# Optimization experiments

Measured on AMD Instinct MI355X. Metric: run time of the kernel, lower is better.

Reference implementation:

```python
import jax, jax.numpy as jnp
import numpy as np

B, R, SR, K, F = 1, 2048, 24, 8, 32
DIST_FREQ = 2   # dist_xyz_freq -> PE dim 2*2*3 = 12
VIEW_FREQ = 4   # num_viewdir_freqs -> PE dim 2*4*3 = 24


def pe(x, n_freqs):
    # positional encoding: concat sin/cos of x * 2^i, flattened over last dim
    fb = (2.0 ** jnp.arange(n_freqs)).astype(x.dtype)          # [L]
    xb = x[..., None] * fb                                      # [..., 3, L]
    enc = jnp.concatenate([jnp.sin(xb), jnp.cos(xb)], axis=-1)  # [..., 3, 2L]
    return enc.reshape(*x.shape[:-1], -1)                       # [..., 3*2L]


def setup_inputs() -> dict:
    key = jax.random.key(0)
    ks = jax.random.split(key, 12)
    s = 0.1  # small init scale for weights
    return {
        'sampled_embedding': jax.random.normal(ks[0], (B, R, SR, K, F), jnp.float32),
        'dists': jax.random.normal(ks[1], (B, R, SR, K, 3), jnp.float32) * 0.1,
        'viewdirs': jax.random.normal(ks[2], (B, R, SR, 3), jnp.float32),
        'pnt_mask': jax.random.randint(ks[3], (B, R, SR, K), 0, 2, jnp.int32),
        'w1': jax.random.normal(ks[4], (F + 2 * DIST_FREQ * 3, 256), jnp.float32) * s,
        'b1': jnp.zeros((256,), jnp.float32),
        'w2': jax.random.normal(ks[5], (256, 256), jnp.float32) * s,
        'b2': jnp.zeros((256,), jnp.float32),
        'wa1': jax.random.normal(ks[6], (256, 256), jnp.float32) * s,
        'ba1': jnp.zeros((256,), jnp.float32),
        'wa2': jax.random.normal(ks[7], (256, 1), jnp.float32) * s,
        'ba2': jnp.zeros((1,), jnp.float32),
        'wc1': jax.random.normal(ks[8], (256 + 2 * VIEW_FREQ * 3, 256), jnp.float32) * s,
        'bc1': jnp.zeros((256,), jnp.float32),
        'wc2': jax.random.normal(ks[9], (256, 3), jnp.float32) * s,
        'bc2': jnp.zeros((3,), jnp.float32),
    }


def reference(sampled_embedding, dists, viewdirs, pnt_mask,
              w1, b1, w2, b2, wa1, ba1, wa2, ba2, wc1, bc1, wc2, bc2):
    mask = pnt_mask.astype(sampled_embedding.dtype)             # [B,R,SR,K]

    # quadric distance kernel -> normalized neighbor weights
    d2 = jnp.sum(dists * dists, axis=-1)                        # [B,R,SR,K]
    w = 1.0 / jnp.clip(d2, 1e-8)
    w = w * mask
    w = w / jnp.clip(jnp.sum(w, axis=-1, keepdims=True), 1e-8)  # agg_weight_norm

    # per-neighbor feature MLP (block1): feat ++ PE(dist_xyz) -> 256 -> 256
    feat_in = jnp.concatenate([sampled_embedding, pe(dists, DIST_FREQ)], axis=-1)
    h = jax.nn.relu(feat_in @ w1 + b1)
    h = jax.nn.relu(h @ w2 + b2)                                # [B,R,SR,K,256]

    # distance-weighted aggregation over neighbors (apply_pnt_mask folded into w)
    agg = jnp.einsum('brsk,brskc->brsc', w, h)                  # [B,R,SR,256]

    # alpha branch + raw2out_density (act_super: softplus(raw - 1))
    ah = jax.nn.relu(agg @ wa1 + ba1)
    density = jax.nn.softplus(ah @ wa2 + ba2 - 1.0)             # [B,R,SR,1]

    # color branch + raw2out_color (widened sigmoid)
    cin = jnp.concatenate([agg, pe(viewdirs, VIEW_FREQ)], axis=-1)
    ch = jax.nn.relu(cin @ wc1 + bc1)
    color = jax.nn.sigmoid(ch @ wc2 + bc2) * (1.0 + 2e-3) - 1e-3  # [B,R,SR,3]

    return jnp.concatenate([density, color], axis=-1)           # [B,R,SR,4]
```

## Files before the change

### kernel.cpp

```cpp
#include <hip/hip_runtime.h>

typedef unsigned short ushort_t;
typedef __bf16 bf16x8 __attribute__((ext_vector_type(8)));
typedef float f32x4 __attribute__((ext_vector_type(4)));

#define NPTS   49152
#define KNBR   8
#define PTS_A  8
#define NBLK_A (NPTS / PTS_A)
#define PTS_B  32
#define NBLK_B (NPTS / PTS_B)

#define W1S_OFF   0
#define W2S_OFF   16384
#define WA1S_OFF  81920
#define WC1S_OFF  147456
#define WA2S_OFF  221184
#define WC2S_OFF  225280
#define WS_WEIGHT 229376
#define AGG_OFF   229376

__device__ __forceinline__ float b2f(ushort_t u) {
    return __builtin_bit_cast(float, ((unsigned)u) << 16);
}
__device__ __forceinline__ ushort_t f2b(float f) {
    unsigned x = __builtin_bit_cast(unsigned, f);
    unsigned r = x + 0x7fffu + ((x >> 16) & 1u);
    return (ushort_t)(r >> 16);
}
__device__ __forceinline__ ushort_t f2bc(float f) {
    unsigned x = __builtin_bit_cast(unsigned, f);
    return (ushort_t)((x + 0x8000u) >> 16);
}

__global__ __launch_bounds__(256) void prep_swizzle(
    const float* __restrict__ w1, const float* __restrict__ w2,
    const float* __restrict__ wa1, const float* __restrict__ wc1,
    const float* __restrict__ wa2, const float* __restrict__ wc2,
    ushort_t* __restrict__ ws)
{
    int idx = blockIdx.x * 256 + threadIdx.x;
    if (idx >= WS_WEIGHT) return;

    if (idx >= WA2S_OFF) {
        int off2 = idx - WA2S_OFF;
        int mat = off2 >> 12;
        int off = off2 & 4095;
        int kb = off >> 7, rem = off & 127;
        int n = rem >> 3, j = rem & 7;
        int k = kb * 8 + j;
        float v = 0.f;
        if (mat == 0) { if (n == 0) v = wa2[k]; }
        else          { if (n < 3)  v = wc2[k * 3 + n]; }
        ws[idx] = f2b(v);
        return;
    }

    const float* src; int off, srcK, base;
    if (idx < W2S_OFF)        { src = w1;  base = W1S_OFF;  off = idx - W1S_OFF;  srcK = 44;  }
    else if (idx < WA1S_OFF)  { src = w2;  base = W2S_OFF;  off = idx - W2S_OFF;  srcK = 256; }
    else if (idx < WC1S_OFF)  { src = wa1; base = WA1S_OFF; off = idx - WA1S_OFF; srcK = 256; }
    else                      { src = wc1; base = WC1S_OFF; off = idx - WC1S_OFF; srcK = 280; }
    int kb  = off >> 11;
    int rem = off & 2047;
    int j = rem >> 8;
    int n = rem & 255;
    int k = kb * 8 + j;
    float v = (k < srcK) ? src[k * 256 + n] : 0.f;
    ws[base + kb * 2048 + n * 8 + j] = f2b(v);
}

__global__ __launch_bounds__(256) void pa_mlp(
    const float* __restrict__ emb, const float* __restrict__ dists,
    const int* __restrict__ mask,  const float* __restrict__ b1,
    const float* __restrict__ b2,  const ushort_t* __restrict__ ws,
    ushort_t* __restrict__ aggg)
{
    __shared__ __align__(16) ushort_t uH1[64 * 264];
    __shared__ __align__(16) float sWraw[64];
    __shared__ __align__(16) float sWn[64];
    ushort_t (*sFeat)[72] = (ushort_t(*)[72])uH1;
    ushort_t (*sH1)[264]  = (ushort_t(*)[264])uH1;

    const int tid  = threadIdx.x;
    const int lane = tid & 63;
    const int wv   = tid >> 6;
    const int n0   = lane & 15;
    const int quad = lane >> 4;
    const int pb   = blockIdx.x * PTS_A;
    const int colB = wv * 64;

    {
        int g0 = blockIdx.x * 2048 + tid * 8;
        int r = tid >> 2, c8 = (tid & 3) * 8;
        float4 f0 = *(const float4*)(emb + g0);
        float4 f1 = *(const float4*)(emb + g0 + 4);
        ushort_t v8[8];
        v8[0] = f2bc(f0.x); v8[1] = f2bc(f0.y); v8[2] = f2bc(f0.z); v8[3] = f2bc(f0.w);
        v8[4] = f2bc(f1.x); v8[5] = f2bc(f1.y); v8[6] = f2bc(f1.z); v8[7] = f2bc(f1.w);
        *(uint4*)&sFeat[r][c8] = *(uint4*)v8;
    }
    if (tid < 64) {
        int gr = pb * KNBR + tid;
        float x = dists[gr * 3 + 0];
        float y = dists[gr * 3 + 1];
        float z = dists[gr * 3 + 2];
        float d2 = x * x + y * y + z * z;
        sWraw[tid] = (float)mask[gr] / fmaxf(d2, 1e-8f);
        float xs[3] = {x, y, z};
        #pragma unroll
        for (int d = 0; d < 3; d++) {
            #pragma unroll
            for (int l = 0; l < 2; l++) {
                float ang = xs[d] * (float)(1 << l);
                sFeat[tid][32 + d * 4 + l]     = f2bc(__sinf(ang));
                sFeat[tid][32 + d * 4 + 2 + l] = f2bc(__cosf(ang));
            }
        }
        #pragma unroll
        for (int c = 44; c < 64; c++) sFeat[tid][c] = 0;
    }
    __syncthreads();
    if (tid < 64) {
        int lp = tid >> 3;
        float s = 0.f;
        #pragma unroll
        for (int k = 0; k < 8; k++) s += sWraw[lp * 8 + k];
        sWn[tid] = sWraw[tid] / fmaxf(s, 1e-8f);
    }

    f32x4 acc[16];
    #pragma unroll
    for (int i = 0; i < 16; i++) acc[i] = (f32x4){0.f, 0.f, 0.f, 0.f};

    #pragma unroll
    for (int ki = 0; ki < 2; ki++) {
        bf16x8 a[4];
        #pragma unroll
        for (int mt = 0; mt < 4; mt++)
            a[mt] = *(const bf16x8*)&sFeat[mt * 16 + n0][ki * 32 + quad * 8];
        const ushort_t* bp = ws + W1S_OFF + ki * 8192 + quad * 2048 + (colB + n0) * 8;
        #pragma unroll
        for (int nt = 0; nt < 4; nt++) {
            bf16x8 b = *(const bf16x8*)(bp + nt * 128);
            #pragma unroll
            for (int mt = 0; mt < 4; mt++)
                acc[mt * 4 + nt] = __builtin_amdgcn_mfma_f32_16x16x32_bf16(a[mt], b, acc[mt * 4 + nt], 0, 0, 0);
        }
    }
    __syncthreads();

    {
        #pragma unroll
        for (int nt = 0; nt < 4; nt++) {
            int col = colB + nt * 16 + n0;
            float bias = b1[col];
            #pragma unroll
            for (int mt = 0; mt < 4; mt++)
                #pragma unroll
                for (int r = 0; r < 4; r++)
                    sH1[mt * 16 + quad * 4 + r][col] = f2bc(fmaxf(acc[mt * 4 + nt][r] + bias, 0.f));
        }
    }
    __syncthreads();

    #pragma unroll
    for (int i = 0; i < 16; i++) acc[i] = (f32x4){0.f, 0.f, 0.f, 0.f};
    #pragma unroll
    for (int ki = 0; ki < 8; ki++) {
        bf16x8 a[4];
        #pragma unroll
        for (int mt = 0; mt < 4; mt++)
            a[mt] = *(const bf16x8*)&sH1[mt * 16 + n0][ki * 32 + quad * 8];
        const ushort_t* bp = ws + W2S_OFF + ki * 8192 + quad * 2048 + (colB + n0) * 8;
        #pragma unroll
        for (int nt = 0; nt < 4; nt++) {
            bf16x8 b = *(const bf16x8*)(bp + nt * 128);
            #pragma unroll
            for (int mt = 0; mt < 4; mt++)
                acc[mt * 4 + nt] = __builtin_amdgcn_mfma_f32_16x16x32_bf16(a[mt], b, acc[mt * 4 + nt], 0, 0, 0);
        }
    }
    {
        #pragma unroll
        for (int mt = 0; mt < 4; mt++) {
            f32x4 wn4 = *(const f32x4*)&sWn[mt * 16 + quad * 4];
            #pragma unroll
            for (int nt = 0; nt < 4; nt++) {
                int col = colB + nt * 16 + n0;
                float bias = b2[col];
                float s = fmaxf(acc[mt * 4 + nt][0] + bias, 0.f) * wn4[0]
                        + fmaxf(acc[mt * 4 + nt][1] + bias, 0.f) * wn4[1]
                        + fmaxf(acc[mt * 4 + nt][2] + bias, 0.f) * wn4[2]
                        + fmaxf(acc[mt * 4 + nt][3] + bias, 0.f) * wn4[3];
                s += __shfl_xor(s, 16);
                if ((quad & 1) == 0) {
                    int pt = pb + 2 * mt + (quad >> 1);
                    aggg[(size_t)pt * 256 + col] = f2bc(s);
                }
            }
        }
    }
}

__global__ __launch_bounds__(256) void pa_branch(
    const float* __restrict__ vdirs,
    const float* __restrict__ ba1v, const float* __restrict__ ba2v,
    const float* __restrict__ bc1v, const float* __restrict__ bc2v,
    const ushort_t* __restrict__ ws, const ushort_t* __restrict__ aggg,
    float* __restrict__ out)
{
    __shared__ __align__(16) ushort_t reg1[32 * 296];
    __shared__ __align__(16) ushort_t reg2[32 * 264];
    ushort_t (*sCin)[296] = (ushort_t(*)[296])reg1;
    ushort_t (*sAh)[264]  = (ushort_t(*)[264])reg1;
    ushort_t (*sCh)[264]  = (ushort_t(*)[264])reg2;

    const int tid  = threadIdx.x;
    const int lane = tid & 63;
    const int wv   = tid >> 6;
    const int n0   = lane & 15;
    const int quad = lane >> 4;
    const int pb   = blockIdx.x * PTS_B;
    const int colB = wv * 64;

    #pragma unroll
    for (int it = 0; it < 4; it++) {
        int idx = (tid + it * 256) * 8;
        uint4 v = *(const uint4*)(aggg + (size_t)pb * 256 + idx);
        *(uint4*)&sCin[idx >> 8][idx & 255] = v;
    }
    #pragma unroll
    for (int it = 0; it < 3; it++) {
        int t = tid + it * 256;
        int p = t / 24, j = t % 24;
        int d = j >> 3, jj = j & 7, l = jj & 3, isc = jj >> 2;
        float ang = vdirs[(pb + p) * 3 + d] * (float)(1 << l);
        sCin[p][256 + j] = f2bc(isc ? __cosf(ang) : __sinf(ang));
    }
    sCin[tid >> 3][280 + (tid & 7)] = 0;
    __syncthreads();

    f32x4 accA[8], accC[8];
    #pragma unroll
    for (int i = 0; i < 8; i++) { accA[i] = (f32x4){0.f, 0.f, 0.f, 0.f}; accC[i] = accA[i]; }

    #pragma unroll
    for (int ki = 0; ki < 8; ki++) {
        bf16x8 a0 = *(const bf16x8*)&sCin[n0][ki * 32 + quad * 8];
        bf16x8 a1 = *(const bf16x8*)&sCin[16 + n0][ki * 32 + quad * 8];
        const ushort_t* bp = ws + WA1S_OFF + ki * 8192 + quad * 2048 + (colB + n0) * 8;
        #pragma unroll
        for (int nt = 0; nt < 4; nt++) {
            bf16x8 b = *(const bf16x8*)(bp + nt * 128);
            accA[nt]     = __builtin_amdgcn_mfma_f32_16x16x32_bf16(a0, b, accA[nt], 0, 0, 0);
            accA[4 + nt] = __builtin_amdgcn_mfma_f32_16x16x32_bf16(a1, b, accA[4 + nt], 0, 0, 0);
        }
    }
    #pragma unroll
    for (int ki = 0; ki < 9; ki++) {
        bf16x8 a0 = *(const bf16x8*)&sCin[n0][ki * 32 + quad * 8];
        bf16x8 a1 = *(const bf16x8*)&sCin[16 + n0][ki * 32 + quad * 8];
        const ushort_t* bp = ws + WC1S_OFF + ki * 8192 + quad * 2048 + (colB + n0) * 8;
        #pragma unroll
        for (int nt = 0; nt < 4; nt++) {
            bf16x8 b = *(const bf16x8*)(bp + nt * 128);
            accC[nt]     = __builtin_amdgcn_mfma_f32_16x16x32_bf16(a0, b, accC[nt], 0, 0, 0);
            accC[4 + nt] = __builtin_amdgcn_mfma_f32_16x16x32_bf16(a1, b, accC[4 + nt], 0, 0, 0);
        }
    }
    __syncthreads();

    #pragma unroll
    for (int nt = 0; nt < 4; nt++) {
        int col = colB + nt * 16 + n0;
        float biasA = ba1v[col];
        float biasC = bc1v[col];
        #pragma unroll
        for (int mt = 0; mt < 2; mt++)
            #pragma unroll
            for (int r = 0; r < 4; r++) {
                int row = mt * 16 + quad * 4 + r;
                sAh[row][col] = f2bc(fmaxf(accA[mt * 4 + nt][r] + biasA, 0.f));
                sCh[row][col] = f2bc(fmaxf(accC[mt * 4 + nt][r] + biasC, 0.f));
            }
    }
    __syncthreads();

    {
        const int isColor = wv >> 1;
        const int baseM   = (wv & 1) * 16;
        const ushort_t* A = isColor ? &sCh[0][0] : &sAh[0][0];
        const ushort_t* B = ws + (isColor ? WC2S_OFF : WA2S_OFF);
        f32x4 acc4 = (f32x4){0.f, 0.f, 0.f, 0.f};
        #pragma unroll
        for (int ki = 0; ki < 8; ki++) {
            bf16x8 a = *(const bf16x8*)(A + (baseM + n0) * 264 + ki * 32 + quad * 8);
            bf16x8 b = *(const bf16x8*)(B + ki * 512 + quad * 128 + n0 * 8);
            acc4 = __builtin_amdgcn_mfma_f32_16x16x32_bf16(a, b, acc4, 0, 0, 0);
        }
        if (!isColor) {
            if (n0 == 0) {
                float ba2s = ba2v[0];
                #pragma unroll
                for (int r = 0; r < 4; r++) {
                    int gp = pb + baseM + quad * 4 + r;
                    float yv = acc4[r] + ba2s - 1.0f;
                    out[(size_t)gp * 4] = (yv > 20.f) ? yv : log1pf(expf(yv));
                }
            }
        } else {
            if (n0 < 3) {
                float bc2s = bc2v[n0];
                #pragma unroll
                for (int r = 0; r < 4; r++) {
                    int gp = pb + baseM + quad * 4 + r;
                    float sig = 1.f / (1.f + expf(-(acc4[r] + bc2s)));
                    out[(size_t)gp * 4 + 1 + n0] = sig * (1.0f + 2e-3f) - 1e-3f;
                }
            }
        }
    }
}

extern "C" void kernel_launch(void* const* d_in, const int* in_sizes, int n_in,
                              void* d_out, int out_size, void* d_ws, size_t ws_size,
                              hipStream_t stream) {
    const float* emb   = (const float*)d_in[0];
    const float* dists = (const float*)d_in[1];
    const float* vdir  = (const float*)d_in[2];
    const int*   mask  = (const int*)d_in[3];
    const float* w1    = (const float*)d_in[4];
    const float* b1    = (const float*)d_in[5];
    const float* w2    = (const float*)d_in[6];
    const float* b2    = (const float*)d_in[7];
    const float* wa1   = (const float*)d_in[8];
    const float* ba1   = (const float*)d_in[9];
    const float* wa2   = (const float*)d_in[10];
    const float* ba2   = (const float*)d_in[11];
    const float* wc1   = (const float*)d_in[12];
    const float* bc1   = (const float*)d_in[13];
    const float* wc2   = (const float*)d_in[14];
    const float* bc2   = (const float*)d_in[15];
    ushort_t* ws  = (ushort_t*)d_ws;
    float*    out = (float*)d_out;

    prep_swizzle<<<dim3((WS_WEIGHT + 255) / 256), dim3(256), 0, stream>>>(
        w1, w2, wa1, wc1, wa2, wc2, ws);
    pa_mlp<<<dim3(NBLK_A), dim3(256), 0, stream>>>(
        emb, dists, mask, b1, b2, ws, ws + AGG_OFF);
    pa_branch<<<dim3(NBLK_B), dim3(256), 0, stream>>>(
        vdir, ba1, ba2, bc1, bc2, ws, ws + AGG_OFF, out);
}
```

Measured before the change: 209.9 us.

## Compact masked neighbors to skip MFMA tiles and fold biases into weights

```diff
diff --git a/kernel.cpp b/kernel.cpp
--- a/kernel.cpp
+++ b/kernel.cpp
@@ -32,10 +32,17 @@
     unsigned x = __builtin_bit_cast(unsigned, f);
     return (ushort_t)((x + 0x8000u) >> 16);
 }
+__device__ __forceinline__ unsigned cvt_pk_bf16(float a, float b) {
+    unsigned r;
+    asm("v_cvt_pk_bf16_f32 %0, %1, %2" : "=v"(r) : "v"(a), "v"(b));
+    return r;
+}
 
 __global__ __launch_bounds__(256) void prep_swizzle(
-    const float* __restrict__ w1, const float* __restrict__ w2,
+    const float* __restrict__ w1, const float* __restrict__ b1,
+    const float* __restrict__ w2,
     const float* __restrict__ wa1, const float* __restrict__ wc1,
+    const float* __restrict__ bc1,
     const float* __restrict__ wa2, const float* __restrict__ wc2,
     ushort_t* __restrict__ ws)
 {
@@ -56,29 +63,33 @@
         return;
     }
 
-    const float* src; int off, srcK, base;
-    if (idx < W2S_OFF)        { src = w1;  base = W1S_OFF;  off = idx - W1S_OFF;  srcK = 44;  }
-    else if (idx < WA1S_OFF)  { src = w2;  base = W2S_OFF;  off = idx - W2S_OFF;  srcK = 256; }
-    else if (idx < WC1S_OFF)  { src = wa1; base = WA1S_OFF; off = idx - WA1S_OFF; srcK = 256; }
-    else                      { src = wc1; base = WC1S_OFF; off = idx - WC1S_OFF; srcK = 280; }
+    const float* src; const float* bias; int off, srcK, base;
+    if (idx < W2S_OFF)        { src = w1;  bias = b1;      base = W1S_OFF;  off = idx - W1S_OFF;  srcK = 44;  }
+    else if (idx < WA1S_OFF)  { src = w2;  bias = nullptr; base = W2S_OFF;  off = idx - W2S_OFF;  srcK = 256; }
+    else if (idx < WC1S_OFF)  { src = wa1; bias = nullptr; base = WA1S_OFF; off = idx - WA1S_OFF; srcK = 256; }
+    else                      { src = wc1; bias = bc1;     base = WC1S_OFF; off = idx - WC1S_OFF; srcK = 280; }
     int kb  = off >> 11;
     int rem = off & 2047;
     int j = rem >> 8;
     int n = rem & 255;
     int k = kb * 8 + j;
-    float v = (k < srcK) ? src[k * 256 + n] : 0.f;
+    float v;
+    if (k < srcK)                 v = src[k * 256 + n];
+    else if (bias && k == srcK)   v = bias[n];
+    else                          v = 0.f;
     ws[base + kb * 2048 + n * 8 + j] = f2b(v);
 }
 
 __global__ __launch_bounds__(256) void pa_mlp(
     const float* __restrict__ emb, const float* __restrict__ dists,
-    const int* __restrict__ mask,  const float* __restrict__ b1,
-    const float* __restrict__ b2,  const ushort_t* __restrict__ ws,
-    ushort_t* __restrict__ aggg)
+    const int* __restrict__ mask,  const float* __restrict__ b2,
+    const ushort_t* __restrict__ ws, ushort_t* __restrict__ aggg)
 {
     __shared__ __align__(16) ushort_t uH1[64 * 264];
-    __shared__ __align__(16) float sWraw[64];
-    __shared__ __align__(16) float sWn[64];
+    __shared__ __align__(16) float sAgg[8][260];
+    __shared__ __align__(16) float sWnS[64];
+    __shared__ __align__(8)  ushort_t sInv[64];
+    __shared__ int sTiles;
     ushort_t (*sFeat)[72] = (ushort_t(*)[72])uH1;
     ushort_t (*sH1)[264]  = (ushort_t(*)[264])uH1;
 
@@ -90,23 +101,32 @@
     const int pb   = blockIdx.x * PTS_A;
     const int colB = wv * 64;
 
+    #pragma unroll
+    for (int i = 0; i < 3; i++) {
+        int idx = tid + i * 256;
+        if (idx < 520) ((f32x4*)sAgg)[idx] = (f32x4){0.f, 0.f, 0.f, 0.f};
+    }
+
     {
         int g0 = blockIdx.x * 2048 + tid * 8;
         int r = tid >> 2, c8 = (tid & 3) * 8;
         float4 f0 = *(const float4*)(emb + g0);
         float4 f1 = *(const float4*)(emb + g0 + 4);
-        ushort_t v8[8];
-        v8[0] = f2bc(f0.x); v8[1] = f2bc(f0.y); v8[2] = f2bc(f0.z); v8[3] = f2bc(f0.w);
-        v8[4] = f2bc(f1.x); v8[5] = f2bc(f1.y); v8[6] = f2bc(f1.z); v8[7] = f2bc(f1.w);
-        *(uint4*)&sFeat[r][c8] = *(uint4*)v8;
+        uint4 u;
+        u.x = cvt_pk_bf16(f0.x, f0.y);
+        u.y = cvt_pk_bf16(f0.z, f0.w);
+        u.z = cvt_pk_bf16(f1.x, f1.y);
+        u.w = cvt_pk_bf16(f1.z, f1.w);
+        *(uint4*)&sFeat[r][c8] = u;
     }
     if (tid < 64) {
         int gr = pb * KNBR + tid;
         float x = dists[gr * 3 + 0];
         float y = dists[gr * 3 + 1];
         float z = dists[gr * 3 + 2];
+        int   m = mask[gr];
         float d2 = x * x + y * y + z * z;
-        sWraw[tid] = (float)mask[gr] / fmaxf(d2, 1e-8f);
+        float wraw = (float)m / fmaxf(d2, 1e-8f);
         float xs[3] = {x, y, z};
         #pragma unroll
         for (int d = 0; d < 3; d++) {
@@ -117,17 +137,30 @@
                 sFeat[tid][32 + d * 4 + 2 + l] = f2bc(__cosf(ang));
             }
         }
-        #pragma unroll
-        for (int c = 44; c < 64; c++) sFeat[tid][c] = 0;
-    }
-    __syncthreads();
-    if (tid < 64) {
-        int lp = tid >> 3;
-        float s = 0.f;
-        #pragma unroll
-        for (int k = 0; k < 8; k++) s += sWraw[lp * 8 + k];
-        sWn[tid] = sWraw[tid] / fmaxf(s, 1e-8f);
-    }
+        sFeat[tid][44] = (ushort_t)0x3f80;
+        #pragma unroll
+        for (int c = 45; c < 64; c++) sFeat[tid][c] = 0;
+
+        float gs = wraw;
+        gs += __shfl_xor(gs, 1);
+        gs += __shfl_xor(gs, 2);
+        gs += __shfl_xor(gs, 4);
+        float wn = wraw / fmaxf(gs, 1e-8f);
+
+        bool act = (m != 0);
+        unsigned long long bm = __ballot(act);
+        int nact = __popcll(bm);
+        int slot = __popcll(bm & ((1ull << lane) - 1ull));
+        if (act) { sInv[slot] = (ushort_t)tid; sWnS[slot] = wn; }
+        if (tid >= nact) { sInv[tid] = 0; sWnS[tid] = 0.f; }
+        if (tid == 0) sTiles = (nact + 15) >> 4;
+    }
+    __syncthreads();
+    const int tiles = __builtin_amdgcn_readfirstlane(sTiles);
+
+    int rowA[4];
+    #pragma unroll
+    for (int mt = 0; mt < 4; mt++) rowA[mt] = sInv[mt * 16 + n0];
 
     f32x4 acc[16];
     #pragma unroll
@@ -138,28 +171,31 @@
         bf16x8 a[4];
         #pragma unroll
         for (int mt = 0; mt < 4; mt++)
-            a[mt] = *(const bf16x8*)&sFeat[mt * 16 + n0][ki * 32 + quad * 8];
+            if (mt < 2 || mt < tiles)
+                a[mt] = *(const bf16x8*)&sFeat[rowA[mt]][ki * 32 + quad * 8];
         const ushort_t* bp = ws + W1S_OFF + ki * 8192 + quad * 2048 + (colB + n0) * 8;
         #pragma unroll
         for (int nt = 0; nt < 4; nt++) {
             bf16x8 b = *(const bf16x8*)(bp + nt * 128);
             #pragma unroll
             for (int mt = 0; mt < 4; mt++)
-                acc[mt * 4 + nt] = __builtin_amdgcn_mfma_f32_16x16x32_bf16(a[mt], b, acc[mt * 4 + nt], 0, 0, 0);
+                if (mt < 2 || mt < tiles)
+                    acc[mt * 4 + nt] = __builtin_amdgcn_mfma_f32_16x16x32_bf16(a[mt], b, acc[mt * 4 + nt], 0, 0, 0);
         }
     }
     __syncthreads();
 
     {
         #pragma unroll
-        for (int nt = 0; nt < 4; nt++) {
-            int col = colB + nt * 16 + n0;
-            float bias = b1[col];
-            #pragma unroll
-            for (int mt = 0; mt < 4; mt++)
+        for (int mt = 0; mt < 4; mt++) {
+            if (!(mt < 2 || mt < tiles)) continue;
+            #pragma unroll
+            for (int nt = 0; nt < 4; nt++) {
+                int col = colB + nt * 16 + n0;
                 #pragma unroll
                 for (int r = 0; r < 4; r++)
-                    sH1[mt * 16 + quad * 4 + r][col] = f2bc(fmaxf(acc[mt * 4 + nt][r] + bias, 0.f));
+                    sH1[mt * 16 + quad * 4 + r][col] = f2bc(fmaxf(acc[mt * 4 + nt][r], 0.f));
+            }
         }
     }
     __syncthreads();
@@ -171,42 +207,57 @@
         bf16x8 a[4];
         #pragma unroll
         for (int mt = 0; mt < 4; mt++)
-            a[mt] = *(const bf16x8*)&sH1[mt * 16 + n0][ki * 32 + quad * 8];
+            if (mt < 2 || mt < tiles)
+                a[mt] = *(const bf16x8*)&sH1[mt * 16 + n0][ki * 32 + quad * 8];
         const ushort_t* bp = ws + W2S_OFF + ki * 8192 + quad * 2048 + (colB + n0) * 8;
         #pragma unroll
         for (int nt = 0; nt < 4; nt++) {
             bf16x8 b = *(const bf16x8*)(bp + nt * 128);
             #pragma unroll
             for (int mt = 0; mt < 4; mt++)
-                acc[mt * 4 + nt] = __builtin_amdgcn_mfma_f32_16x16x32_bf16(a[mt], b, acc[mt * 4 + nt], 0, 0, 0);
+                if (mt < 2 || mt < tiles)
+                    acc[mt * 4 + nt] = __builtin_amdgcn_mfma_f32_16x16x32_bf16(a[mt], b, acc[mt * 4 + nt], 0, 0, 0);
         }
     }
     {
+        float b2v[4];
+        #pragma unroll
+        for (int nt = 0; nt < 4; nt++) b2v[nt] = b2[colB + nt * 16 + n0];
         #pragma unroll
         for (int mt = 0; mt < 4; mt++) {
-            f32x4 wn4 = *(const f32x4*)&sWn[mt * 16 + quad * 4];
+            if (!(mt < 2 || mt < tiles)) continue;
+            f32x4 wn4 = *(const f32x4*)&sWnS[mt * 16 + quad * 4];
+            ushort4 iv = *(const ushort4*)&sInv[mt * 16 + quad * 4];
+            int p0 = iv.x >> 3, p1 = iv.y >> 3, p2 = iv.z >> 3, p3 = iv.w >> 3;
             #pragma unroll
             for (int nt = 0; nt < 4; nt++) {
                 int col = colB + nt * 16 + n0;
-                float bias = b2[col];
-                float s = fmaxf(acc[mt * 4 + nt][0] + bias, 0.f) * wn4[0]
-                        + fmaxf(acc[mt * 4 + nt][1] + bias, 0.f) * wn4[1]
-                        + fmaxf(acc[mt * 4 + nt][2] + bias, 0.f) * wn4[2]
-                        + fmaxf(acc[mt * 4 + nt][3] + bias, 0.f) * wn4[3];
-                s += __shfl_xor(s, 16);
-                if ((quad & 1) == 0) {
-                    int pt = pb + 2 * mt + (quad >> 1);
-                    aggg[(size_t)pt * 256 + col] = f2bc(s);
-                }
-            }
-        }
+                atomicAdd(&sAgg[p0][col], fmaxf(acc[mt * 4 + nt][0] + b2v[nt], 0.f) * wn4[0]);
+                atomicAdd(&sAgg[p1][col], fmaxf(acc[mt * 4 + nt][1] + b2v[nt], 0.f) * wn4[1]);
+                atomicAdd(&sAgg[p2][col], fmaxf(acc[mt * 4 + nt][2] + b2v[nt], 0.f) * wn4[2]);
+                atomicAdd(&sAgg[p3][col], fmaxf(acc[mt * 4 + nt][3] + b2v[nt], 0.f) * wn4[3]);
+            }
+        }
+    }
+    __syncthreads();
+    {
+        int p  = tid >> 5;
+        int c0 = (tid & 31) * 8;
+        f32x4 a0 = *(const f32x4*)&sAgg[p][c0];
+        f32x4 a1 = *(const f32x4*)&sAgg[p][c0 + 4];
+        uint4 u;
+        u.x = cvt_pk_bf16(a0[0], a0[1]);
+        u.y = cvt_pk_bf16(a0[2], a0[3]);
+        u.z = cvt_pk_bf16(a1[0], a1[1]);
+        u.w = cvt_pk_bf16(a1[2], a1[3]);
+        *(uint4*)(aggg + (size_t)(pb + p) * 256 + c0) = u;
     }
 }
 
 __global__ __launch_bounds__(256) void pa_branch(
     const float* __restrict__ vdirs,
     const float* __restrict__ ba1v, const float* __restrict__ ba2v,
-    const float* __restrict__ bc1v, const float* __restrict__ bc2v,
+    const float* __restrict__ bc2v,
     const ushort_t* __restrict__ ws, const ushort_t* __restrict__ aggg,
     float* __restrict__ out)
 {
@@ -238,7 +289,7 @@
         float ang = vdirs[(pb + p) * 3 + d] * (float)(1 << l);
         sCin[p][256 + j] = f2bc(isc ? __cosf(ang) : __sinf(ang));
     }
-    sCin[tid >> 3][280 + (tid & 7)] = 0;
+    sCin[tid >> 3][280 + (tid & 7)] = ((tid & 7) == 0) ? (ushort_t)0x3f80 : (ushort_t)0;
     __syncthreads();
 
     f32x4 accA[8], accC[8];
@@ -275,14 +326,13 @@
     for (int nt = 0; nt < 4; nt++) {
         int col = colB + nt * 16 + n0;
         float biasA = ba1v[col];
-        float biasC = bc1v[col];
         #pragma unroll
         for (int mt = 0; mt < 2; mt++)
             #pragma unroll
             for (int r = 0; r < 4; r++) {
                 int row = mt * 16 + quad * 4 + r;
                 sAh[row][col] = f2bc(fmaxf(accA[mt * 4 + nt][r] + biasA, 0.f));
-                sCh[row][col] = f2bc(fmaxf(accC[mt * 4 + nt][r] + biasC, 0.f));
+                sCh[row][col] = f2bc(fmaxf(accC[mt * 4 + nt][r], 0.f));
             }
     }
     __syncthreads();
@@ -346,9 +396,9 @@
     float*    out = (float*)d_out;
 
     prep_swizzle<<<dim3((WS_WEIGHT + 255) / 256), dim3(256), 0, stream>>>(
-        w1, w2, wa1, wc1, wa2, wc2, ws);
+        w1, b1, w2, wa1, wc1, bc1, wa2, wc2, ws);
     pa_mlp<<<dim3(NBLK_A), dim3(256), 0, stream>>>(
-        emb, dists, mask, b1, b2, ws, ws + AGG_OFF);
+        emb, dists, mask, b2, ws, ws + AGG_OFF);
     pa_branch<<<dim3(NBLK_B), dim3(256), 0, stream>>>(
-        vdir, ba1, ba2, bc1, bc2, ws, ws + AGG_OFF, out);
-}
+        vdir, ba1, ba2, bc2, ws, ws + AGG_OFF, out);
+}
```

New measurement: 533.3 us. +154.1%, slower.

## Fuse alpha and color first-layer GEMMs with biases folded into weights

Applied to the files above, without the earlier changes.

```diff
diff --git a/kernel.cpp b/kernel.cpp
--- a/kernel.cpp
+++ b/kernel.cpp
@@ -13,12 +13,11 @@
 
 #define W1S_OFF   0
 #define W2S_OFF   16384
-#define WA1S_OFF  81920
-#define WC1S_OFF  147456
-#define WA2S_OFF  221184
-#define WC2S_OFF  225280
-#define WS_WEIGHT 229376
-#define AGG_OFF   229376
+#define WHS_OFF   81920
+#define WA2S_OFF  229376
+#define WC2S_OFF  233472
+#define WS_WEIGHT 237568
+#define AGG_OFF   237568
 
 __device__ __forceinline__ float b2f(ushort_t u) {
     return __builtin_bit_cast(float, ((unsigned)u) << 16);
@@ -35,7 +34,8 @@
 
 __global__ __launch_bounds__(256) void prep_swizzle(
     const float* __restrict__ w1, const float* __restrict__ w2,
-    const float* __restrict__ wa1, const float* __restrict__ wc1,
+    const float* __restrict__ wa1, const float* __restrict__ ba1,
+    const float* __restrict__ wc1, const float* __restrict__ bc1,
     const float* __restrict__ wa2, const float* __restrict__ wc2,
     ushort_t* __restrict__ ws)
 {
@@ -55,12 +55,28 @@
         ws[idx] = f2b(v);
         return;
     }
-
+    if (idx >= WHS_OFF) {
+        int off = idx - WHS_OFF;
+        int kb  = off >> 12;
+        int rem = off & 4095;
+        int j = rem >> 9;
+        int n = rem & 511;
+        int k = kb * 8 + j;
+        float v = 0.f;
+        if (n < 256) {
+            if (k < 256)       v = wa1[k * 256 + n];
+            else if (k == 280) v = ba1[n];
+        } else {
+            int nc = n - 256;
+            if (k < 280)       v = wc1[k * 256 + nc];
+            else if (k == 280) v = bc1[nc];
+        }
+        ws[WHS_OFF + kb * 4096 + n * 8 + j] = f2b(v);
+        return;
+    }
     const float* src; int off, srcK, base;
-    if (idx < W2S_OFF)        { src = w1;  base = W1S_OFF;  off = idx - W1S_OFF;  srcK = 44;  }
-    else if (idx < WA1S_OFF)  { src = w2;  base = W2S_OFF;  off = idx - W2S_OFF;  srcK = 256; }
-    else if (idx < WC1S_OFF)  { src = wa1; base = WA1S_OFF; off = idx - WA1S_OFF; srcK = 256; }
-    else                      { src = wc1; base = WC1S_OFF; off = idx - WC1S_OFF; srcK = 280; }
+    if (idx < W2S_OFF) { src = w1; base = W1S_OFF; off = idx - W1S_OFF; srcK = 44;  }
+    else               { src = w2; base = W2S_OFF; off = idx - W2S_OFF; srcK = 256; }
     int kb  = off >> 11;
     int rem = off & 2047;
     int j = rem >> 8;
@@ -76,11 +92,11 @@
     const float* __restrict__ b2,  const ushort_t* __restrict__ ws,
     ushort_t* __restrict__ aggg)
 {
-    __shared__ __align__(16) ushort_t uH1[64 * 264];
+    __shared__ __align__(16) ushort_t uH1[64 * 266];
     __shared__ __align__(16) float sWraw[64];
     __shared__ __align__(16) float sWn[64];
-    ushort_t (*sFeat)[72] = (ushort_t(*)[72])uH1;
-    ushort_t (*sH1)[264]  = (ushort_t(*)[264])uH1;
+    ushort_t (*sFeat)[74] = (ushort_t(*)[74])uH1;
+    ushort_t (*sH1)[266]  = (ushort_t(*)[266])uH1;
 
     const int tid  = threadIdx.x;
     const int lane = tid & 63;
@@ -205,16 +221,13 @@
 
 __global__ __launch_bounds__(256) void pa_branch(
     const float* __restrict__ vdirs,
-    const float* __restrict__ ba1v, const float* __restrict__ ba2v,
-    const float* __restrict__ bc1v, const float* __restrict__ bc2v,
+    const float* __restrict__ ba2v, const float* __restrict__ bc2v,
     const ushort_t* __restrict__ ws, const ushort_t* __restrict__ aggg,
     float* __restrict__ out)
 {
-    __shared__ __align__(16) ushort_t reg1[32 * 296];
-    __shared__ __align__(16) ushort_t reg2[32 * 264];
-    ushort_t (*sCin)[296] = (ushort_t(*)[296])reg1;
-    ushort_t (*sAh)[264]  = (ushort_t(*)[264])reg1;
-    ushort_t (*sCh)[264]  = (ushort_t(*)[264])reg2;
+    __shared__ __align__(16) ushort_t shm[32 * 530];
+    ushort_t (*sCin)[298] = (ushort_t(*)[298])shm;
+    ushort_t (*sH)[530]   = (ushort_t(*)[530])shm;
 
     const int tid  = threadIdx.x;
     const int lane = tid & 63;
@@ -222,7 +235,7 @@
     const int n0   = lane & 15;
     const int quad = lane >> 4;
     const int pb   = blockIdx.x * PTS_B;
-    const int colB = wv * 64;
+    const int colB2 = wv * 128;
 
     #pragma unroll
     for (int it = 0; it < 4; it++) {
@@ -238,64 +251,49 @@
         float ang = vdirs[(pb + p) * 3 + d] * (float)(1 << l);
         sCin[p][256 + j] = f2bc(isc ? __cosf(ang) : __sinf(ang));
     }
-    sCin[tid >> 3][280 + (tid & 7)] = 0;
-    __syncthreads();
-
-    f32x4 accA[8], accC[8];
-    #pragma unroll
-    for (int i = 0; i < 8; i++) { accA[i] = (f32x4){0.f, 0.f, 0.f, 0.f}; accC[i] = accA[i]; }
-
-    #pragma unroll
-    for (int ki = 0; ki < 8; ki++) {
-        bf16x8 a0 = *(const bf16x8*)&sCin[n0][ki * 32 + quad * 8];
-        bf16x8 a1 = *(const bf16x8*)&sCin[16 + n0][ki * 32 + quad * 8];
-        const ushort_t* bp = ws + WA1S_OFF + ki * 8192 + quad * 2048 + (colB + n0) * 8;
-        #pragma unroll
-        for (int nt = 0; nt < 4; nt++) {
-            bf16x8 b = *(const bf16x8*)(bp + nt * 128);
-            accA[nt]     = __builtin_amdgcn_mfma_f32_16x16x32_bf16(a0, b, accA[nt], 0, 0, 0);
-            accA[4 + nt] = __builtin_amdgcn_mfma_f32_16x16x32_bf16(a1, b, accA[4 + nt], 0, 0, 0);
-        }
-    }
+    sCin[tid >> 3][280 + (tid & 7)] = ((tid & 7) == 0) ? (ushort_t)0x3f80 : (ushort_t)0;
+    __syncthreads();
+
+    f32x4 acc[16];
+    #pragma unroll
+    for (int i = 0; i < 16; i++) acc[i] = (f32x4){0.f, 0.f, 0.f, 0.f};
+
     #pragma unroll
     for (int ki = 0; ki < 9; ki++) {
         bf16x8 a0 = *(const bf16x8*)&sCin[n0][ki * 32 + quad * 8];
         bf16x8 a1 = *(const bf16x8*)&sCin[16 + n0][ki * 32 + quad * 8];
-        const ushort_t* bp = ws + WC1S_OFF + ki * 8192 + quad * 2048 + (colB + n0) * 8;
-        #pragma unroll
-        for (int nt = 0; nt < 4; nt++) {
+        const ushort_t* bp = ws + WHS_OFF + ki * 16384 + quad * 4096 + (colB2 + n0) * 8;
+        #pragma unroll
+        for (int nt = 0; nt < 8; nt++) {
             bf16x8 b = *(const bf16x8*)(bp + nt * 128);
-            accC[nt]     = __builtin_amdgcn_mfma_f32_16x16x32_bf16(a0, b, accC[nt], 0, 0, 0);
-            accC[4 + nt] = __builtin_amdgcn_mfma_f32_16x16x32_bf16(a1, b, accC[4 + nt], 0, 0, 0);
-        }
-    }
-    __syncthreads();
-
-    #pragma unroll
-    for (int nt = 0; nt < 4; nt++) {
-        int col = colB + nt * 16 + n0;
-        float biasA = ba1v[col];
-        float biasC = bc1v[col];
-        #pragma unroll
-        for (int mt = 0; mt < 2; mt++)
-            #pragma unroll
-            for (int r = 0; r < 4; r++) {
-                int row = mt * 16 + quad * 4 + r;
-                sAh[row][col] = f2bc(fmaxf(accA[mt * 4 + nt][r] + biasA, 0.f));
-                sCh[row][col] = f2bc(fmaxf(accC[mt * 4 + nt][r] + biasC, 0.f));
-            }
+            acc[nt]     = __builtin_amdgcn_mfma_f32_16x16x32_bf16(a0, b, acc[nt], 0, 0, 0);
+            acc[8 + nt] = __builtin_amdgcn_mfma_f32_16x16x32_bf16(a1, b, acc[8 + nt], 0, 0, 0);
+        }
+    }
+    __syncthreads();
+
+    {
+        #pragma unroll
+        for (int nt = 0; nt < 8; nt++) {
+            int col = colB2 + nt * 16 + n0;
+            #pragma unroll
+            for (int mt = 0; mt < 2; mt++)
+                #pragma unroll
+                for (int r = 0; r < 4; r++)
+                    sH[mt * 16 + quad * 4 + r][col] = f2bc(fmaxf(acc[mt * 8 + nt][r], 0.f));
+        }
     }
     __syncthreads();
 
     {
         const int isColor = wv >> 1;
         const int baseM   = (wv & 1) * 16;
-        const ushort_t* A = isColor ? &sCh[0][0] : &sAh[0][0];
+        const int cOff    = isColor ? 256 : 0;
         const ushort_t* B = ws + (isColor ? WC2S_OFF : WA2S_OFF);
         f32x4 acc4 = (f32x4){0.f, 0.f, 0.f, 0.f};
         #pragma unroll
         for (int ki = 0; ki < 8; ki++) {
-            bf16x8 a = *(const bf16x8*)(A + (baseM + n0) * 264 + ki * 32 + quad * 8);
+            bf16x8 a = *(const bf16x8*)&sH[baseM + n0][cOff + ki * 32 + quad * 8];
             bf16x8 b = *(const bf16x8*)(B + ki * 512 + quad * 128 + n0 * 8);
             acc4 = __builtin_amdgcn_mfma_f32_16x16x32_bf16(a, b, acc4, 0, 0, 0);
         }
@@ -346,9 +344,9 @@
     float*    out = (float*)d_out;
 
     prep_swizzle<<<dim3((WS_WEIGHT + 255) / 256), dim3(256), 0, stream>>>(
-        w1, w2, wa1, wc1, wa2, wc2, ws);
+        w1, w2, wa1, ba1, wc1, bc1, wa2, wc2, ws);
     pa_mlp<<<dim3(NBLK_A), dim3(256), 0, stream>>>(
         emb, dists, mask, b1, b2, ws, ws + AGG_OFF);
     pa_branch<<<dim3(NBLK_B), dim3(256), 0, stream>>>(
-        vdir, ba1, ba2, bc1, bc2, ws, ws + AGG_OFF, out);
-}
+        vdir, ba2, bc2, ws, ws + AGG_OFF, out);
+}
```

Result: slower. 284.7 us (+35.7%).
